# Kernel tuning notes

Measured on AMD Instinct MI355X. Metric: run time of the kernel, lower is better.

Reference implementation:

```python
import jax, jax.numpy as jnp
import numpy as np

K = 2
N_NODES = 100_000
N_EDGES = 1_600_000
STATIC_F = 16
DYN_F = 32
EDGE_F = 8
IN_F = EDGE_F + 2 * STATIC_F + 2 * DYN_F  # 104
HID_F = 2 * DYN_F  # 64


def setup_inputs() -> dict:
    key = jax.random.key(0)
    ks = jax.random.split(key, 9)
    x_s = jax.random.normal(ks[0], (N_NODES, STATIC_F), dtype=jnp.float32)
    x_t = jax.random.normal(ks[1], (N_NODES, DYN_F), dtype=jnp.float32)
    edge_index = jax.random.randint(ks[2], (2, N_EDGES), 0, N_NODES, dtype=jnp.int64 if jax.config.jax_enable_x64 else jnp.int32)
    edge_attr = jax.random.normal(ks[3], (N_EDGES, EDGE_F), dtype=jnp.float32)
    W1 = jax.random.normal(ks[4], (IN_F, HID_F), dtype=jnp.float32) / np.sqrt(IN_F)
    b1 = jnp.zeros((HID_F,), dtype=jnp.float32)
    W2 = jax.random.normal(ks[5], (HID_F, DYN_F), dtype=jnp.float32) / np.sqrt(HID_F)
    b2 = jnp.zeros((DYN_F,), dtype=jnp.float32)
    F = jax.random.normal(ks[6], (K + 1, DYN_F, DYN_F), dtype=jnp.float32) / np.sqrt(DYN_F)
    return {"x_s": x_s, "x_t": x_t, "edge_index": edge_index, "edge_attr": edge_attr,
            "W1": W1, "b1": b1, "W2": W2, "b2": b2, "F": F}


def reference(x_s, x_t, edge_index, edge_attr, W1, b1, W2, b2, F):
    row, col = edge_index[0], edge_index[1]
    num_nodes = x_t.shape[0]
    # filter_matrix[0] (Linear, no bias); F[k] stored as [in, out]
    out = x_t @ F[0]
    xs_row = x_s[row]  # static gathers are loop-invariant
    xs_col = x_s[col]
    for k in range(K):
        mask = jnp.sum(out, axis=1) != 0  # [N]
        edge_mask = (mask[row] | mask[col]).astype(out.dtype)[:, None]  # [E,1]
        out_row = out[row]
        out_col = out[col]
        e_ij = jnp.concatenate([xs_row, xs_col, out_row, out_col, edge_attr], axis=1)  # [E,104]
        w_ij = jax.nn.relu(e_ij @ W1 + b1) @ W2 + b2  # [E,32]
        # normalize per edge; NaN (zero-norm) -> 0, matching masked_fill_
        nrm = jnp.linalg.norm(w_ij, axis=1, keepdims=True)
        w_ij = jnp.where(nrm > 0, w_ij / jnp.where(nrm > 0, nrm, 1.0), 0.0)
        # with_gradient: (x_j - x_i) * w_ij; zero out edges failing the mask
        shift = (out_col - out_row) * w_ij * edge_mask
        scattered = jax.ops.segment_sum(shift, col, num_segments=num_nodes)
        out = out + scattered @ F[k + 1]
    return out
```

## Files before the change

kernel.cpp:

```cpp
#include <hip/hip_runtime.h>

#define NN 100000
#define NE 1600000
#define SF 16
#define DF 32
#define EFT 8
#define HF 64

typedef __attribute__((ext_vector_type(8))) _Float16 half8;
typedef __attribute__((ext_vector_type(4))) _Float16 half4v;
typedef __attribute__((ext_vector_type(8))) short short8;
typedef __attribute__((ext_vector_type(4))) float floatx4;

__global__ __launch_bounds__(256) void hist_kernel(const int* __restrict__ ei,
                                                   int* __restrict__ deg) {
  int e = blockIdx.x * 256 + threadIdx.x;
  if (e < NE) atomicAdd(&deg[ei[NE + e]], 1);
}

__global__ __launch_bounds__(256) void scan1_kernel(const int* __restrict__ deg,
                                                    int* __restrict__ cur,
                                                    int* __restrict__ bsums) {
  __shared__ int ts[256];
  int tid = threadIdx.x;
  int base = blockIdx.x * 1024 + tid * 4;
  int v[4];
#pragma unroll
  for (int q = 0; q < 4; ++q) v[q] = (base + q < NN) ? deg[base + q] : 0;
  int s = v[0] + v[1] + v[2] + v[3];
  ts[tid] = s;
  __syncthreads();
  for (int off = 1; off < 256; off <<= 1) {
    int t = (tid >= off) ? ts[tid - off] : 0;
    __syncthreads();
    ts[tid] += t;
    __syncthreads();
  }
  int excl = ts[tid] - s;
  if (tid == 255) bsums[blockIdx.x] = ts[255];
  int run = excl;
#pragma unroll
  for (int q = 0; q < 4; ++q) {
    if (base + q < NN) cur[base + q] = run;
    run += v[q];
  }
}

__global__ __launch_bounds__(256) void scan3_kernel(int* __restrict__ cur,
                                                    const int* __restrict__ bsums) {
  int i = blockIdx.x * 256 + threadIdx.x;
  int g = blockIdx.x >> 2;
  int pref = 0;
  for (int q = 0; q < g; ++q) pref += bsums[q];
  if (i < NN) cur[i] += pref;
}

__global__ __launch_bounds__(256) void setup_kernel(
    const float* __restrict__ W1, const float* __restrict__ W2,
    _Float16* __restrict__ WpreT, _Float16* __restrict__ w2pk,
    _Float16* __restrict__ w1epk,
    float4* __restrict__ scattered4, int* __restrict__ deg) {
  int gid = blockIdx.x * 256 + threadIdx.x;
  if (gid < 800000) {
    float4 z = {0.f, 0.f, 0.f, 0.f};
    scattered4[gid] = z;
  }
  if (gid < NN) deg[gid] = 0;
  if (gid < 128 * 64) {
    int col = gid >> 6, k = gid & 63;
    int j = col & 63;
    bool bh = col >= 64;
    float v = 0.f;
    if (k < 16) v = W1[((bh ? 16 : 0) + k) * HF + j];
    else if (k < 48) v = W1[((bh ? 64 : 32) + (k - 16)) * HF + j];
    WpreT[gid] = (_Float16)v;
  }
  if (gid < 2048) {
    int lane = gid >> 5, idx = gid & 31;
    int kt = idx >> 4, nt = (idx >> 3) & 1, q = idx & 7;
    int kgrp = (lane >> 4) & 3, lcol = lane & 15;
    w2pk[gid] = (_Float16)W2[(kt * 32 + kgrp * 8 + q) * DF + nt * 16 + lcol];
  } else if (gid < 4096) {
    int id = gid - 2048;
    int lane = id >> 5, idx = id & 31;
    int jblk = idx >> 3, t = idx & 7;
    float v = (lane < 16) ? W1[(96 + t) * HF + jblk * 16 + lane] : 0.f;
    w1epk[id] = (_Float16)v;
  }
}

__global__ __launch_bounds__(256) void fill_kernel(
    const int* __restrict__ ei, const float* __restrict__ ea,
    int* __restrict__ cur, char* __restrict__ recs) {
  int e = blockIdx.x * 256 + threadIdx.x;
  int r = ei[e];
  int c = ei[NE + e];
  int pos = atomicAdd(&cur[c], 1);
  const float4* p = (const float4*)(ea + (size_t)e * EFT);
  float4 v0 = p[0], v1 = p[1];
  union { _Float16 h[2]; int i; } p01, p23, p45, p67;
  p01.h[0] = (_Float16)v0.x; p01.h[1] = (_Float16)v0.y;
  p23.h[0] = (_Float16)v0.z; p23.h[1] = (_Float16)v0.w;
  p45.h[0] = (_Float16)v1.x; p45.h[1] = (_Float16)v1.y;
  p67.h[0] = (_Float16)v1.z; p67.h[1] = (_Float16)v1.w;
  int2* rp = (int2*)(recs + (size_t)pos * 24);
  int2 a = {r, c};
  int2 b = {p01.i, p23.i};
  int2 d = {p45.i, p67.i};
  rp[0] = a; rp[1] = b; rp[2] = d;
}

__global__ __launch_bounds__(256) void init_kernel(
    const float* __restrict__ x_t, const float* __restrict__ F0,
    float* __restrict__ out, _Float16* __restrict__ outb,
    float* __restrict__ sums) {
  int n = blockIdx.x * 256 + threadIdx.x;
  if (n >= NN) return;
  float x[DF];
  const float4* xr = reinterpret_cast<const float4*>(x_t + (size_t)n * DF);
#pragma unroll
  for (int q = 0; q < 8; ++q) {
    float4 v = xr[q];
    x[4*q+0]=v.x; x[4*q+1]=v.y; x[4*q+2]=v.z; x[4*q+3]=v.w;
  }
  float4* orow = reinterpret_cast<float4*>(out + (size_t)n * DF);
  _Float16* ob = outb + (size_t)n * DF;
  float s = 0.f;
#pragma unroll
  for (int q = 0; q < 8; ++q) {
    float4 acc = {0.f, 0.f, 0.f, 0.f};
#pragma unroll
    for (int i = 0; i < DF; ++i) {
      float xi = x[i];
      acc.x = fmaf(xi, F0[i*DF + 4*q+0], acc.x);
      acc.y = fmaf(xi, F0[i*DF + 4*q+1], acc.y);
      acc.z = fmaf(xi, F0[i*DF + 4*q+2], acc.z);
      acc.w = fmaf(xi, F0[i*DF + 4*q+3], acc.w);
    }
    orow[q] = acc;
    s += acc.x + acc.y + acc.z + acc.w;
    half4v pk = {(_Float16)acc.x, (_Float16)acc.y, (_Float16)acc.z, (_Float16)acc.w};
    *(half4v*)(ob + 4*q) = pk;
  }
  sums[n] = s;
}

__global__ __launch_bounds__(256, 4) void pre_kernel(
    const float* __restrict__ x_s, const _Float16* __restrict__ outb,
    const _Float16* __restrict__ WpreT, _Float16* __restrict__ ABh) {
  __shared__ _Float16 wlds[128][72];
  int tid = threadIdx.x;
  for (int t = tid; t < 1024; t += 256) {
    int colr = t >> 3, kc = t & 7;
    *(half8*)(&wlds[colr][kc * 8]) = *(const half8*)(WpreT + colr * 64 + kc * 8);
  }
  __syncthreads();

  int lcol = tid & 15, kgrp = (tid >> 4) & 3, wid = tid >> 6;
  int nodebase = blockIdx.x * 64 + wid * 16;
  int nodeA = nodebase + lcol;

  half8 a0 = {}, a1 = {};
  if (nodeA < NN) {
    const _Float16* obp = outb + (size_t)nodeA * DF;
    if (kgrp < 2) {
      const float4* p = (const float4*)(x_s + (size_t)nodeA * SF);
      float4 v0 = p[kgrp * 2], v1 = p[kgrp * 2 + 1];
      a0[0]=(_Float16)v0.x; a0[1]=(_Float16)v0.y;
      a0[2]=(_Float16)v0.z; a0[3]=(_Float16)v0.w;
      a0[4]=(_Float16)v1.x; a0[5]=(_Float16)v1.y;
      a0[6]=(_Float16)v1.z; a0[7]=(_Float16)v1.w;
      a1 = *(const half8*)(obp + 16 + kgrp * 8);
    } else if (kgrp == 2) {
      a0 = *(const half8*)(obp + 0);
    } else {
      a0 = *(const half8*)(obp + 8);
    }
  }

  floatx4 acc[8];
#pragma unroll
  for (int nt = 0; nt < 8; ++nt) {
    half8 b0 = *(const half8*)(&wlds[nt * 16 + lcol][kgrp * 8]);
    half8 b1v = *(const half8*)(&wlds[nt * 16 + lcol][32 + kgrp * 8]);
    floatx4 c = {0.f, 0.f, 0.f, 0.f};
    c = __builtin_amdgcn_mfma_f32_16x16x32_f16(a0, b0, c, 0, 0, 0);
    c = __builtin_amdgcn_mfma_f32_16x16x32_f16(a1, b1v, c, 0, 0, 0);
    acc[nt] = c;
  }

#pragma unroll
  for (int rr = 0; rr < 4; ++rr) {
    int node = nodebase + kgrp * 4 + rr;
    if (node < NN) {
      _Float16* dst = ABh + (size_t)node * 128;
#pragma unroll
      for (int nt = 0; nt < 8; ++nt)
        dst[nt * 16 + lcol] = (_Float16)acc[nt][rr];
    }
  }
}

__global__ __launch_bounds__(256, 4) void edge_kernel(
    const _Float16* __restrict__ ABh, const _Float16* __restrict__ outb,
    const float* __restrict__ sums, const char* __restrict__ recs,
    const float* __restrict__ b1, const float* __restrict__ b2,
    const _Float16* __restrict__ w2pk, const _Float16* __restrict__ w1epk,
    float* __restrict__ scattered) {
  __shared__ union { _Float16 h[256][72]; float sh[9472]; } u;
  __shared__ int scol[256];
  __shared__ unsigned short l0[256], l1[256];
  __shared__ int wbase[4];
  __shared__ int cnt;

  int tid = threadIdx.x;
  int bbase = blockIdx.x * 256;
  int i = bbase + tid;
  if (tid == 0) cnt = 0;
  int lcol = tid & 15, kgrp = (tid >> 4) & 3, wid = tid >> 6;
  int lane = tid & 63;

  const int2* rp = (const int2*)(recs + (size_t)i * 24);
  int2 ra = rp[0], rb = rp[1], rd = rp[2];
  int r = ra.x;
  int c = ra.y;
  int4 eai = {rb.x, rb.y, rd.x, rd.y};
  scol[tid] = c;
  float s_r = sums[r], s_c = sums[c];

  const _Float16* wpp = w2pk + (size_t)lane * 32;
  half8 w2f00 = *(const half8*)(wpp);
  half8 w2f01 = *(const half8*)(wpp + 8);
  half8 w2f10 = *(const half8*)(wpp + 16);
  half8 w2f11 = *(const half8*)(wpp + 24);
  float b2c0 = b2[lcol], b2c1 = b2[16 + lcol];

  const _Float16* wep = w1epk + (size_t)lane * 32;
  half8 wA0 = *(const half8*)(wep);
  half8 wA1 = *(const half8*)(wep + 8);
  half8 wA2 = *(const half8*)(wep + 16);
  half8 wA3 = *(const half8*)(wep + 24);
  const float4* b1f4 = (const float4*)b1;
  float4 b1q0 = b1f4[0 + kgrp];
  float4 b1q1 = b1f4[4 + kgrp];
  float4 b1q2 = b1f4[8 + kgrp];
  float4 b1q3 = b1f4[12 + kgrp];
  bool lo16 = lane < 16;
#pragma unroll
  for (int g = 0; g < 4; ++g) {
    int src = g * 16 + lcol;
    int4 t;
    t.x = __shfl(eai.x, src, 64);
    t.y = __shfl(eai.y, src, 64);
    t.z = __shfl(eai.z, src, 64);
    t.w = __shfl(eai.w, src, 64);
    half8 zz = {};
    half8 bg = lo16 ? __builtin_bit_cast(half8, t) : zz;
    int erow = wid * 64 + g * 16 + lcol;
    _Float16* hrow = &u.h[erow][kgrp * 4];
    {
      floatx4 cc = {b1q0.x, b1q0.y, b1q0.z, b1q0.w};
      cc = __builtin_amdgcn_mfma_f32_16x16x32_f16(wA0, bg, cc, 0, 0, 0);
      half4v h4 = {(_Float16)cc[0], (_Float16)cc[1], (_Float16)cc[2], (_Float16)cc[3]};
      *(half4v*)(hrow + 0) = h4;
    }
    {
      floatx4 cc = {b1q1.x, b1q1.y, b1q1.z, b1q1.w};
      cc = __builtin_amdgcn_mfma_f32_16x16x32_f16(wA1, bg, cc, 0, 0, 0);
      half4v h4 = {(_Float16)cc[0], (_Float16)cc[1], (_Float16)cc[2], (_Float16)cc[3]};
      *(half4v*)(hrow + 16) = h4;
    }
    {
      floatx4 cc = {b1q2.x, b1q2.y, b1q2.z, b1q2.w};
      cc = __builtin_amdgcn_mfma_f32_16x16x32_f16(wA2, bg, cc, 0, 0, 0);
      half4v h4 = {(_Float16)cc[0], (_Float16)cc[1], (_Float16)cc[2], (_Float16)cc[3]};
      *(half4v*)(hrow + 32) = h4;
    }
    {
      floatx4 cc = {b1q3.x, b1q3.y, b1q3.z, b1q3.w};
      cc = __builtin_amdgcn_mfma_f32_16x16x32_f16(wA3, bg, cc, 0, 0, 0);
      half4v h4 = {(_Float16)cc[0], (_Float16)cc[1], (_Float16)cc[2], (_Float16)cc[3]};
      *(half4v*)(hrow + 48) = h4;
    }
  }

  const _Float16* ar = ABh + (size_t)r * 128;
  const _Float16* bc = ABh + (size_t)c * 128 + 64;
#pragma unroll 4
  for (int q = 0; q < 8; ++q) {
    half8 a = *(const half8*)(ar + q * 8);
    half8 b = *(const half8*)(bc + q * 8);
    half8 w = *(const half8*)(&u.h[tid][q * 8]);
    half8 s = a + b + w;
    short8 sb = __builtin_bit_cast(short8, s);
    short8 m = sb >> 15;
    sb = sb & ~m;
    *(short8*)(&u.h[tid][q * 8]) = sb;
  }

  floatx4 acc[4][2];
#pragma unroll
  for (int g = 0; g < 4; ++g) {
    int erow = wid * 64 + g * 16 + lcol;
    half8 a0 = *(const half8*)(&u.h[erow][kgrp * 8]);
    half8 a1 = *(const half8*)(&u.h[erow][32 + kgrp * 8]);
    floatx4 c0 = {b2c0, b2c0, b2c0, b2c0};
    floatx4 c1 = {b2c1, b2c1, b2c1, b2c1};
    c0 = __builtin_amdgcn_mfma_f32_16x16x32_f16(a0, w2f00, c0, 0, 0, 0);
    c0 = __builtin_amdgcn_mfma_f32_16x16x32_f16(a1, w2f10, c0, 0, 0, 0);
    c1 = __builtin_amdgcn_mfma_f32_16x16x32_f16(a0, w2f01, c1, 0, 0, 0);
    c1 = __builtin_amdgcn_mfma_f32_16x16x32_f16(a1, w2f11, c1, 0, 0, 0);
    acc[g][0] = c0;
    acc[g][1] = c1;
  }

  __syncthreads();

#pragma unroll
  for (int g = 0; g < 4; ++g) {
#pragma unroll
    for (int rr = 0; rr < 4; ++rr) {
      int e = wid * 64 + g * 16 + kgrp * 4 + rr;
      u.sh[e * 37 + lcol]      = acc[g][0][rr];
      u.sh[e * 37 + 16 + lcol] = acc[g][1][rr];
    }
  }

  {
    float o2[32];
    float nsq = 0.f;
#pragma unroll
    for (int j = 0; j < 32; ++j) {
      float v = u.sh[tid * 37 + j];
      o2[j] = v;
      nsq = fmaf(v, v, nsq);
    }
    float ms = (nsq > 0.f) ? rsqrtf(nsq) : 0.f;
    if (s_r == 0.f && s_c == 0.f) ms = 0.f;
    const half8* orp = (const half8*)(outb + (size_t)r * DF);
    const half8* ocp = (const half8*)(outb + (size_t)c * DF);
#pragma unroll
    for (int q = 0; q < 4; ++q) {
      half8 av = orp[q], bv = ocp[q];
#pragma unroll
      for (int jj = 0; jj < 8; ++jj)
        u.sh[tid * 37 + q * 8 + jj] =
            ((float)bv[jj] - (float)av[jj]) * o2[q * 8 + jj] * ms;
    }
  }
  __syncthreads();

  int c_self = scol[tid];
  bool head = (tid == 0 || scol[tid - 1] != c_self);
  unsigned long long m = __ballot(head);
  if (lane == 0) wbase[wid] = atomicAdd(&cnt, (int)__popcll(m));
  __syncthreads();
  if (head) {
    int idx = wbase[wid] + (int)__popcll(m & ((1ull << lane) - 1ull));
    int t1 = tid + 1;
    while (t1 < 256 && scol[t1] == c_self) ++t1;
    l0[idx] = (unsigned short)tid;
    l1[idx] = (unsigned short)t1;
  }
  __syncthreads();
  int nr = cnt;
  for (int task = tid; task < nr * 32; task += 256) {
    int rid = task >> 5, j = task & 31;
    int t0 = l0[rid], t1 = l1[rid];
    float s = 0.f;
    for (int t = t0; t < t1; ++t) s += u.sh[t * 37 + j];
    unsafeAtomicAdd(&scattered[(size_t)scol[t0] * DF + j], s);
  }
}

__global__ __launch_bounds__(256) void node_kernel(
    float* __restrict__ out, float* __restrict__ scattered,
    const float* __restrict__ Fk, _Float16* __restrict__ outb,
    float* __restrict__ sums) {
  int n = blockIdx.x * 256 + threadIdx.x;
  if (n >= NN) return;
  float s[DF];
  float4* sp = reinterpret_cast<float4*>(scattered + (size_t)n * DF);
#pragma unroll
  for (int q = 0; q < 8; ++q) {
    float4 v = sp[q];
    s[4*q+0]=v.x; s[4*q+1]=v.y; s[4*q+2]=v.z; s[4*q+3]=v.w;
  }
  float4* op = reinterpret_cast<float4*>(out + (size_t)n * DF);
  _Float16* ob = outb + (size_t)n * DF;
  float ssum = 0.f;
#pragma unroll
  for (int q = 0; q < 8; ++q) {
    float4 acc = op[q];
#pragma unroll
    for (int i = 0; i < DF; ++i) {
      float si = s[i];
      acc.x = fmaf(si, Fk[i*DF + 4*q+0], acc.x);
      acc.y = fmaf(si, Fk[i*DF + 4*q+1], acc.y);
      acc.z = fmaf(si, Fk[i*DF + 4*q+2], acc.z);
      acc.w = fmaf(si, Fk[i*DF + 4*q+3], acc.w);
    }
    op[q] = acc;
    ssum += acc.x + acc.y + acc.z + acc.w;
    half4v pk = {(_Float16)acc.x, (_Float16)acc.y, (_Float16)acc.z, (_Float16)acc.w};
    *(half4v*)(ob + 4*q) = pk;
  }
  sums[n] = ssum;
  float4 z = {0.f, 0.f, 0.f, 0.f};
#pragma unroll
  for (int q = 0; q < 8; ++q) sp[q] = z;
}

extern "C" void kernel_launch(void* const* d_in, const int* in_sizes, int n_in,
                              void* d_out, int out_size, void* d_ws, size_t ws_size,
                              hipStream_t stream) {
  const float* x_s = (const float*)d_in[0];
  const float* x_t = (const float*)d_in[1];
  const int*   ei  = (const int*)d_in[2];
  const float* ea  = (const float*)d_in[3];
  const float* W1  = (const float*)d_in[4];
  const float* b1  = (const float*)d_in[5];
  const float* W2  = (const float*)d_in[6];
  const float* b2  = (const float*)d_in[7];
  const float* F   = (const float*)d_in[8];

  float* out = (float*)d_out;
  char* ws = (char*)d_ws;
  float*     scattered = (float*)(ws);
  _Float16*  ABh       = (_Float16*)(ws + 12800000);
  _Float16*  outb      = (_Float16*)(ws + 38400000);
  float*     sums      = (float*)(ws + 44800000);
  char*      recs      = (char*)(ws + 45200000);
  int*       deg       = (int*)(ws + 83600000);
  int*       cur       = (int*)(ws + 84000000);
  int*       bsums     = (int*)(ws + 84400000);
  _Float16*  WpreT     = (_Float16*)(ws + 84410000);
  _Float16*  w2pk      = (_Float16*)(ws + 84430000);
  _Float16*  w1epk     = (_Float16*)(ws + 84440000);

  dim3 blk(256);
  dim3 grid_e(NE / 256);
  dim3 grid_n((NN + 255) / 256);
  dim3 grid_p((NN + 63) / 64);
  int nscan = (NN + 1023) / 1024;

  setup_kernel<<<3125, blk, 0, stream>>>(W1, W2, WpreT, w2pk, w1epk,
                                         (float4*)scattered, deg);
  hist_kernel<<<grid_e, blk, 0, stream>>>(ei, deg);
  scan1_kernel<<<nscan, blk, 0, stream>>>(deg, cur, bsums);
  scan3_kernel<<<grid_n, blk, 0, stream>>>(cur, bsums);
  fill_kernel<<<grid_e, blk, 0, stream>>>(ei, ea, cur, recs);

  init_kernel<<<grid_n, blk, 0, stream>>>(x_t, F, out, outb, sums);

  for (int k = 0; k < 2; ++k) {
    pre_kernel<<<grid_p, blk, 0, stream>>>(x_s, outb, WpreT, ABh);
    edge_kernel<<<grid_e, blk, 0, stream>>>(ABh, outb, sums, recs, b1, b2,
                                            w2pk, w1epk, scattered);
    node_kernel<<<grid_n, blk, 0, stream>>>(out, scattered,
                                            F + (size_t)(k + 1) * DF * DF,
                                            outb, sums);
  }
}
```

Before: 451.1 us.

## Hoist gathered loads earlier and XOR-swizzle the hidden-activation LDS tile

The edge kernel now issues the row/col gathers of the precomputed node projections at kernel start, and the out-feature gathers before the barrier, so their latency overlaps the first-layer MFMA work. The half-precision hidden tile drops its padding in favour of an XOR swizzle on 16-byte granules, and the float staging stride shrinks from 37 to 33, which lowers LDS use and aims to avoid bank conflicts. The cost is higher register pressure from holding 24 half8 vectors live, which could reduce occupancy under the (256,4) launch bound.

```diff
diff --git a/kernel.cpp b/kernel.cpp
--- a/kernel.cpp
+++ b/kernel.cpp
@@ -11,6 +11,11 @@
 typedef __attribute__((ext_vector_type(4))) _Float16 half4v;
 typedef __attribute__((ext_vector_type(8))) short short8;
 typedef __attribute__((ext_vector_type(4))) float floatx4;
+
+__device__ inline int hswz(int row, int halfoff) {
+  int gran = halfoff >> 3, sub = halfoff & 7;
+  return row * 64 + ((gran ^ (row & 7)) << 3) + sub;
+}
 
 __global__ __launch_bounds__(256) void hist_kernel(const int* __restrict__ ei,
                                                    int* __restrict__ deg) {
@@ -207,7 +212,7 @@
     const float* __restrict__ b1, const float* __restrict__ b2,
     const _Float16* __restrict__ w2pk, const _Float16* __restrict__ w1epk,
     float* __restrict__ scattered) {
-  __shared__ union { _Float16 h[256][72]; float sh[9472]; } u;
+  __shared__ union { _Float16 h[256 * 64]; float sh[256 * 33]; } u;
   __shared__ int scol[256];
   __shared__ unsigned short l0[256], l1[256];
   __shared__ int wbase[4];
@@ -228,11 +233,14 @@
   scol[tid] = c;
   float s_r = sums[r], s_c = sums[c];
 
-  const _Float16* wpp = w2pk + (size_t)lane * 32;
-  half8 w2f00 = *(const half8*)(wpp);
-  half8 w2f01 = *(const half8*)(wpp + 8);
-  half8 w2f10 = *(const half8*)(wpp + 16);
-  half8 w2f11 = *(const half8*)(wpp + 24);
+  half8 Ar[8], Bc[8];
+  {
+    const half8* arp = (const half8*)(ABh + (size_t)r * 128);
+    const half8* bcp = (const half8*)(ABh + (size_t)c * 128 + 64);
+#pragma unroll
+    for (int q = 0; q < 8; ++q) { Ar[q] = arp[q]; Bc[q] = bcp[q]; }
+  }
+
   float b2c0 = b2[lcol], b2c1 = b2[16 + lcol];
 
   const _Float16* wep = w1epk + (size_t)lane * 32;
@@ -257,53 +265,54 @@
     half8 zz = {};
     half8 bg = lo16 ? __builtin_bit_cast(half8, t) : zz;
     int erow = wid * 64 + g * 16 + lcol;
-    _Float16* hrow = &u.h[erow][kgrp * 4];
     {
       floatx4 cc = {b1q0.x, b1q0.y, b1q0.z, b1q0.w};
       cc = __builtin_amdgcn_mfma_f32_16x16x32_f16(wA0, bg, cc, 0, 0, 0);
       half4v h4 = {(_Float16)cc[0], (_Float16)cc[1], (_Float16)cc[2], (_Float16)cc[3]};
-      *(half4v*)(hrow + 0) = h4;
+      *(half4v*)(&u.h[hswz(erow, 0 * 16 + kgrp * 4)]) = h4;
     }
     {
       floatx4 cc = {b1q1.x, b1q1.y, b1q1.z, b1q1.w};
       cc = __builtin_amdgcn_mfma_f32_16x16x32_f16(wA1, bg, cc, 0, 0, 0);
       half4v h4 = {(_Float16)cc[0], (_Float16)cc[1], (_Float16)cc[2], (_Float16)cc[3]};
-      *(half4v*)(hrow + 16) = h4;
+      *(half4v*)(&u.h[hswz(erow, 1 * 16 + kgrp * 4)]) = h4;
     }
     {
       floatx4 cc = {b1q2.x, b1q2.y, b1q2.z, b1q2.w};
       cc = __builtin_amdgcn_mfma_f32_16x16x32_f16(wA2, bg, cc, 0, 0, 0);
       half4v h4 = {(_Float16)cc[0], (_Float16)cc[1], (_Float16)cc[2], (_Float16)cc[3]};
-      *(half4v*)(hrow + 32) = h4;
+      *(half4v*)(&u.h[hswz(erow, 2 * 16 + kgrp * 4)]) = h4;
     }
     {
       floatx4 cc = {b1q3.x, b1q3.y, b1q3.z, b1q3.w};
       cc = __builtin_amdgcn_mfma_f32_16x16x32_f16(wA3, bg, cc, 0, 0, 0);
       half4v h4 = {(_Float16)cc[0], (_Float16)cc[1], (_Float16)cc[2], (_Float16)cc[3]};
-      *(half4v*)(hrow + 48) = h4;
-    }
-  }
-
-  const _Float16* ar = ABh + (size_t)r * 128;
-  const _Float16* bc = ABh + (size_t)c * 128 + 64;
-#pragma unroll 4
+      *(half4v*)(&u.h[hswz(erow, 3 * 16 + kgrp * 4)]) = h4;
+    }
+  }
+
+#pragma unroll
   for (int q = 0; q < 8; ++q) {
-    half8 a = *(const half8*)(ar + q * 8);
-    half8 b = *(const half8*)(bc + q * 8);
-    half8 w = *(const half8*)(&u.h[tid][q * 8]);
-    half8 s = a + b + w;
+    int idx = hswz(tid, q * 8);
+    half8 w = *(const half8*)(&u.h[idx]);
+    half8 s = Ar[q] + Bc[q] + w;
     short8 sb = __builtin_bit_cast(short8, s);
     short8 m = sb >> 15;
     sb = sb & ~m;
-    *(short8*)(&u.h[tid][q * 8]) = sb;
-  }
-
+    *(short8*)(&u.h[idx]) = sb;
+  }
+
+  const _Float16* wpp = w2pk + (size_t)lane * 32;
+  half8 w2f00 = *(const half8*)(wpp);
+  half8 w2f01 = *(const half8*)(wpp + 8);
+  half8 w2f10 = *(const half8*)(wpp + 16);
+  half8 w2f11 = *(const half8*)(wpp + 24);
   floatx4 acc[4][2];
 #pragma unroll
   for (int g = 0; g < 4; ++g) {
     int erow = wid * 64 + g * 16 + lcol;
-    half8 a0 = *(const half8*)(&u.h[erow][kgrp * 8]);
-    half8 a1 = *(const half8*)(&u.h[erow][32 + kgrp * 8]);
+    half8 a0 = *(const half8*)(&u.h[hswz(erow, kgrp * 8)]);
+    half8 a1 = *(const half8*)(&u.h[hswz(erow, 32 + kgrp * 8)]);
     floatx4 c0 = {b2c0, b2c0, b2c0, b2c0};
     floatx4 c1 = {b2c1, b2c1, b2c1, b2c1};
     c0 = __builtin_amdgcn_mfma_f32_16x16x32_f16(a0, w2f00, c0, 0, 0, 0);
@@ -314,6 +323,14 @@
     acc[g][1] = c1;
   }
 
+  half8 Or[4], Oc[4];
+  {
+    const half8* orp = (const half8*)(outb + (size_t)r * DF);
+    const half8* ocp = (const half8*)(outb + (size_t)c * DF);
+#pragma unroll
+    for (int q = 0; q < 4; ++q) { Or[q] = orp[q]; Oc[q] = ocp[q]; }
+  }
+
   __syncthreads();
 
 #pragma unroll
@@ -321,8 +338,8 @@
 #pragma unroll
     for (int rr = 0; rr < 4; ++rr) {
       int e = wid * 64 + g * 16 + kgrp * 4 + rr;
-      u.sh[e * 37 + lcol]      = acc[g][0][rr];
-      u.sh[e * 37 + 16 + lcol] = acc[g][1][rr];
+      u.sh[e * 33 + lcol]      = acc[g][0][rr];
+      u.sh[e * 33 + 16 + lcol] = acc[g][1][rr];
     }
   }
 
@@ -331,21 +348,18 @@
     float nsq = 0.f;
 #pragma unroll
     for (int j = 0; j < 32; ++j) {
-      float v = u.sh[tid * 37 + j];
+      float v = u.sh[tid * 33 + j];
       o2[j] = v;
       nsq = fmaf(v, v, nsq);
     }
     float ms = (nsq > 0.f) ? rsqrtf(nsq) : 0.f;
     if (s_r == 0.f && s_c == 0.f) ms = 0.f;
-    const half8* orp = (const half8*)(outb + (size_t)r * DF);
-    const half8* ocp = (const half8*)(outb + (size_t)c * DF);
 #pragma unroll
     for (int q = 0; q < 4; ++q) {
-      half8 av = orp[q], bv = ocp[q];
 #pragma unroll
       for (int jj = 0; jj < 8; ++jj)
-        u.sh[tid * 37 + q * 8 + jj] =
-            ((float)bv[jj] - (float)av[jj]) * o2[q * 8 + jj] * ms;
+        u.sh[tid * 33 + q * 8 + jj] =
+            ((float)Oc[q][jj] - (float)Or[q][jj]) * o2[q * 8 + jj] * ms;
     }
   }
   __syncthreads();
@@ -368,7 +382,7 @@
     int rid = task >> 5, j = task & 31;
     int t0 = l0[rid], t1 = l1[rid];
     float s = 0.f;
-    for (int t = t0; t < t1; ++t) s += u.sh[t * 37 + j];
+    for (int t = t0; t < t1; ++t) s += u.sh[t * 33 + j];
     unsafeAtomicAdd(&scattered[(size_t)scol[t0] * DF + j], s);
   }
 }
```

Measured after the change: 441.8 us (median of 2 runs). 1.02x faster.
